# Kernel tuning notes

Measured on AMD Instinct MI355X. Metric: run time of the kernel, lower is better.

## Reference

```python
import jax, jax.numpy as jnp
import numpy as np

NB_HEAD = 16
SIZE_PER_HEAD = 64
D_MODEL = NB_HEAD * SIZE_PER_HEAD  # 1024
B, L = 2, 2048
NEG_BIG = 1e12


def setup_inputs() -> dict:
    key = jax.random.key(0)
    ks = jax.random.split(key, 8)
    return {
        "Q_seq": jax.random.normal(ks[0], (B, L, D_MODEL), dtype=jnp.float32),
        "K_seq": jax.random.normal(ks[1], (B, L, D_MODEL), dtype=jnp.float32),
        "V_seq": jax.random.normal(ks[2], (B, L, D_MODEL), dtype=jnp.float32),
        "q_len": jax.random.randint(ks[3], (B, 1), 1, L, dtype=jnp.int32),
        "v_len": jax.random.randint(ks[4], (B, 1), 1, L, dtype=jnp.int32),
        "WQ": jax.random.normal(ks[5], (D_MODEL, D_MODEL), dtype=jnp.float32) * 0.02,
        "WK": jax.random.normal(ks[6], (D_MODEL, D_MODEL), dtype=jnp.float32) * 0.02,
        "WV": jax.random.normal(ks[7], (D_MODEL, D_MODEL), dtype=jnp.float32) * 0.02,
    }


def _len_mask(lens, length, dtype):
    # Keras code: mask = 1 - cumsum(one_hot(len, L)) -> 1 for pos < len, 0 otherwise
    return (jnp.arange(length)[None, :] < lens).astype(dtype)  # [B, L]


def reference(Q_seq, K_seq, V_seq, q_len, v_len, WQ, WK, WV):
    Bq, Lq, _ = Q_seq.shape
    Lk = K_seq.shape[1]
    # QKV projections, split heads: [B, H, L, D]
    q = (Q_seq @ WQ).reshape(Bq, Lq, NB_HEAD, SIZE_PER_HEAD).transpose(0, 2, 1, 3)
    k = (K_seq @ WK).reshape(Bq, Lk, NB_HEAD, SIZE_PER_HEAD).transpose(0, 2, 1, 3)
    v = (V_seq @ WV).reshape(Bq, Lk, NB_HEAD, SIZE_PER_HEAD).transpose(0, 2, 1, 3)
    # scaled dot-product scores [B, H, Lq, Lk]
    scores = jnp.einsum("bhqd,bhkd->bhqk", q, k) / np.float32(SIZE_PER_HEAD ** 0.5)
    # additive key-length mask (V_len), matching Mask(..., 'add')
    kmask = _len_mask(v_len, Lk, scores.dtype)  # [B, Lk]
    scores = scores - (1.0 - kmask)[:, None, None, :] * np.float32(NEG_BIG)
    A = jax.nn.softmax(scores, axis=-1)
    # attention output, merge heads: [B, Lq, H*D]
    O = jnp.einsum("bhqk,bhkd->bqhd", A, v).reshape(Bq, Lq, D_MODEL)
    # multiplicative query-length mask (Q_len), matching Mask(..., 'mul')
    qmask = _len_mask(q_len, Lq, O.dtype)  # [B, Lq]
    return O * qmask[:, :, None]
```

## Files before the change

### kernel.cpp

```cpp
#include <hip/hip_runtime.h>
#include <cstddef>

#define NB_HEAD 16
#define HEAD_DIM 64
#define D_MODEL 1024
#define BATCH 2
#define SEQ 2048
#define MROWS (BATCH * SEQ)
#define NSPLIT 2

typedef __bf16 bf16x8 __attribute__((ext_vector_type(8)));
typedef __bf16 bf16x4 __attribute__((ext_vector_type(4)));
typedef __bf16 bf16x2 __attribute__((ext_vector_type(2)));
typedef float  f32x4  __attribute__((ext_vector_type(4)));

#define XEL ((size_t)MROWS * D_MODEL)
#define WEL ((size_t)D_MODEL * D_MODEL)

#define QSCALE 0.18033688011112042f

static __device__ __forceinline__ size_t xchunk(int row, int k) {
    return ((size_t)(row >> 4) * 32 + (k >> 5)) * 512 + ((k >> 3) & 3) * 128 + (row & 15) * 8 + (k & 7);
}
static __device__ __forceinline__ size_t qkbase(int bh, int row16, int dc) {
    return ((size_t)(bh * 128 + row16) * 2 + dc) * 512;
}
static __device__ __forceinline__ size_t qkelem(int bh, int row, int d) {
    return qkbase(bh, row >> 4, d >> 5) + ((d >> 3) & 3) * 128 + (row & 15) * 8 + (d & 7);
}
static __device__ __forceinline__ size_t vbase(int bh, int d16, int kc) {
    return ((size_t)(bh * 4 + d16) * 64 + kc) * 512;
}
static __device__ __forceinline__ size_t velem(int bh, int d, int key) {
    return vbase(bh, d >> 4, key >> 5) + ((key >> 3) & 3) * 128 + (d & 15) * 8 + (key & 7);
}

static __device__ __forceinline__ void split_bf16(float x, __bf16& h, __bf16& l) {
    h = (__bf16)x;
    l = (__bf16)(x - (float)h);
}

static __device__ __forceinline__ void gload_lds16(const __bf16* g, __bf16* l) {
    __builtin_amdgcn_global_load_lds((const __attribute__((address_space(1))) void*)g,
                                     (__attribute__((address_space(3))) void*)l,
                                     16, 0, 0);
}

__global__ __launch_bounds__(256) void conv_wt_kernel(
    const float* __restrict__ W0, const float* __restrict__ W1,
    const float* __restrict__ W2,
    __bf16* __restrict__ hi, __bf16* __restrict__ lo)
{
    __shared__ float tile[64][65];
    const int t  = threadIdx.x;
    const int k0 = blockIdx.x * 64;
    const int n0 = blockIdx.y * 64;
    const int z  = blockIdx.z;
    const float* W = (z == 0) ? W0 : ((z == 1) ? W1 : W2);
    __bf16* hz = hi + (size_t)z * WEL;
    __bf16* lz = lo + (size_t)z * WEL;

    #pragma unroll
    for (int p = 0; p < 4; ++p) {
        const int e = (p * 256 + t) * 4;
        const int r = e >> 6, c = e & 63;
        const float4 v = *(const float4*)(W + (size_t)(k0 + r) * D_MODEL + n0 + c);
        tile[r][c] = v.x; tile[r][c + 1] = v.y; tile[r][c + 2] = v.z; tile[r][c + 3] = v.w;
    }
    __syncthreads();
    #pragma unroll
    for (int p = 0; p < 4; ++p) {
        const int e = (p * 256 + t) * 4;
        const int n = e >> 6, kc = e & 63;
        __bf16 h[4], l[4];
        #pragma unroll
        for (int u = 0; u < 4; ++u) split_bf16(tile[kc + u][n], h[u], l[u]);
        const size_t a = xchunk(n0 + n, k0 + kc);
        *(bf16x4*)(hz + a) = (bf16x4){h[0], h[1], h[2], h[3]};
        *(bf16x4*)(lz + a) = (bf16x4){l[0], l[1], l[2], l[3]};
    }
}

__global__ __launch_bounds__(256) void conv_x_kernel(
    const float* __restrict__ X0, const float* __restrict__ X1,
    const float* __restrict__ X2,
    const int* __restrict__ q_len, const int* __restrict__ v_len,
    __bf16* __restrict__ xhi, __bf16* __restrict__ xlo)
{
    const int z = blockIdx.y;
    const size_t e = ((size_t)blockIdx.x * 256 + threadIdx.x) * 8;
    const int l = (int)(e >> 10), k = (int)(e & 1023);
    const int bb = l >> 11, lb = l & (SEQ - 1);
    const int len = (z == 0) ? q_len[bb] : v_len[bb];
    if (lb >= ((len + 127) & ~127)) return;

    const float* X = (z == 0) ? X0 : ((z == 1) ? X1 : X2);
    const float4 v0 = *(const float4*)(X + e);
    const float4 v1 = *(const float4*)(X + e + 4);
    const float xs[8] = {v0.x, v0.y, v0.z, v0.w, v1.x, v1.y, v1.z, v1.w};
    bf16x8 h8, l8;
    #pragma unroll
    for (int u = 0; u < 8; ++u) { __bf16 h_, l_; split_bf16(xs[u], h_, l_); h8[u] = h_; l8[u] = l_; }
    const size_t a = z * XEL + xchunk(l, k);
    *(bf16x8*)(xhi + a) = h8;
    *(bf16x8*)(xlo + a) = l8;
}

__global__ __launch_bounds__(256, 3) void proj_mfma_kernel(
    const __bf16* __restrict__ Xhi, const __bf16* __restrict__ Xlo,
    const __bf16* __restrict__ Wchi, const __bf16* __restrict__ Wclo,
    const int* __restrict__ q_len, const int* __restrict__ v_len,
    __bf16* __restrict__ qch, __bf16* __restrict__ qcl,
    __bf16* __restrict__ kch, __bf16* __restrict__ kcl,
    __bf16* __restrict__ vch, __bf16* __restrict__ vcl)
{
    __shared__ __align__(16) __bf16 lds[2][24][512];

    const int t    = threadIdx.x;
    const int wave = t >> 6, lane = t & 63;
    const int li   = lane & 15, grp = lane >> 4;
    const int wm   = wave >> 1, wn = wave & 1;
    const int m0   = blockIdx.x * 128;
    const int n0   = blockIdx.y * 64;
    const int z    = blockIdx.z;
    const int bb   = m0 >> 11;
    const int l0   = m0 & (SEQ - 1);
    const int need = (z == 0) ? q_len[bb] : v_len[bb];
    if (l0 >= need) return;

    const __bf16* Xh = Xhi + z * XEL;
    const __bf16* Xl = Xlo + z * XEL;
    const __bf16* Wh = Wchi + z * WEL;
    const __bf16* Wl = Wclo + z * WEL;

    const __bf16* gs[6];
    #pragma unroll
    for (int u = 0; u < 6; ++u) {
        const int c = u * 4 + wave;
        const __bf16* src;
        int idx;
        if (c < 8)       { src = Xh; idx = (m0 >> 4) + c; }
        else if (c < 16) { src = Xl; idx = (m0 >> 4) + (c - 8); }
        else if (c < 20) { src = Wh; idx = (n0 >> 4) + (c - 16); }
        else             { src = Wl; idx = (n0 >> 4) + (c - 20); }
        gs[u] = src + (size_t)idx * 32 * 512 + (size_t)lane * 8;
    }

    auto STAGE = [&](int buf, int kc) {
        #pragma unroll
        for (int u = 0; u < 6; ++u)
            gload_lds16(gs[u] + (size_t)kc * 512, &lds[buf][u * 4 + wave][0]);
    };

    f32x4 acc[4][2] = {};

    STAGE(0, 0);
    __syncthreads();

    #pragma unroll 2
    for (int kc = 0; kc < 32; ++kc) {
        const int cur = kc & 1;
        if (kc < 31) STAGE(cur ^ 1, kc + 1);

        bf16x8 ah[4], al4[4], bh2[2], bl2[2];
        #pragma unroll
        for (int i = 0; i < 4; ++i) {
            ah[i]  = *(const bf16x8*)&lds[cur][(wm << 2) + i][lane * 8];
            al4[i] = *(const bf16x8*)&lds[cur][8 + (wm << 2) + i][lane * 8];
        }
        #pragma unroll
        for (int j = 0; j < 2; ++j) {
            bh2[j] = *(const bf16x8*)&lds[cur][16 + (wn << 1) + j][lane * 8];
            bl2[j] = *(const bf16x8*)&lds[cur][20 + (wn << 1) + j][lane * 8];
        }
        #pragma unroll
        for (int j = 0; j < 2; ++j) {
            #pragma unroll
            for (int i = 0; i < 4; ++i) {
                acc[i][j] = __builtin_amdgcn_mfma_f32_16x16x32_bf16(ah[i],  bh2[j], acc[i][j], 0, 0, 0);
                acc[i][j] = __builtin_amdgcn_mfma_f32_16x16x32_bf16(ah[i],  bl2[j], acc[i][j], 0, 0, 0);
                acc[i][j] = __builtin_amdgcn_mfma_f32_16x16x32_bf16(al4[i], bh2[j], acc[i][j], 0, 0, 0);
            }
        }
        __syncthreads();
    }

    #pragma unroll
    for (int j = 0; j < 2; ++j) {
        const int cg = n0 + wn * 32 + j * 16 + li;
        const int hd = cg >> 6, d = cg & 63;
        const int bhI = bb * NB_HEAD + hd;
        #pragma unroll
        for (int i = 0; i < 4; ++i) {
            #pragma unroll
            for (int r = 0; r < 4; ++r) {
                const int rg = m0 + wm * 64 + i * 16 + grp * 4 + r;
                const int lg = rg & (SEQ - 1);
                __bf16 h_, l_;
                if (z == 0) {
                    split_bf16(acc[i][j][r] * QSCALE, h_, l_);
                    const size_t a = qkelem(bhI, lg, d);
                    qch[a] = h_; qcl[a] = l_;
                } else if (z == 1) {
                    split_bf16(acc[i][j][r], h_, l_);
                    const size_t a = qkelem(bhI, lg, d);
                    kch[a] = h_; kcl[a] = l_;
                } else {
                    split_bf16(acc[i][j][r], h_, l_);
                    const size_t a = velem(bhI, d, lg);
                    vch[a] = h_; vcl[a] = l_;
                }
            }
        }
    }
}

__global__ __launch_bounds__(256, 2) void attn_mfma_kernel(
    const __bf16* __restrict__ qch, const __bf16* __restrict__ qcl,
    const __bf16* __restrict__ kch, const __bf16* __restrict__ kcl,
    const __bf16* __restrict__ vch, const __bf16* __restrict__ vcl,
    const int* __restrict__ q_len, const int* __restrict__ v_len,
    float* __restrict__ Opart, float* __restrict__ Mbuf, float* __restrict__ Lbuf)
{
    __shared__ __align__(16) __bf16 Ps[128][72];

    const int t = threadIdx.x;
    const int wq = t >> 6, lane = t & 63;
    const int grp = lane >> 4, li = lane & 15;
    const int hh = blockIdx.x;
    const int split = blockIdx.y & (NSPLIT - 1);
    const int q0 = (blockIdx.y >> 1) * 128;
    const int b  = blockIdx.z;
    const int qlen = q_len[b], vlen = v_len[b];
    const int bh = b * NB_HEAD + hh;
    const int qbase = q0 + wq * 32;

    if (qbase >= qlen) return;

    bf16x8 onesv;
    #pragma unroll
    for (int u = 0; u < 8; ++u) onesv[u] = (__bf16)1.0f;

    bf16x8 qh[2][2], ql[2][2];
    #pragma unroll
    for (int s = 0; s < 2; ++s)
        #pragma unroll
        for (int ks = 0; ks < 2; ++ks) {
            const size_t a = qkbase(bh, (qbase >> 4) + s, ks) + lane * 8;
            qh[s][ks] = *(const bf16x8*)(qch + a);
            ql[s][ks] = *(const bf16x8*)(qcl + a);
        }

    f32x4 O[2][4] = {};
    float m_s[2] = {-1e30f, -1e30f};
    float l_s[2][4];
    #pragma unroll
    for (int s = 0; s < 2; ++s)
        #pragma unroll
        for (int r = 0; r < 4; ++r) l_s[s][r] = 0.f;

    const int nktT = (vlen + 63) >> 6;
    const int half = (nktT + NSPLIT - 1) / NSPLIT;
    const int tBeg = split * half;
    const int tEnd = (nktT < tBeg + half) ? nktT : (tBeg + half);

    for (int tt = tBeg; tt < tEnd; ++tt) {
        const int k0 = tt * 64;
        const bool full = (k0 + 64 <= vlen);

        f32x4 sacc[2][4] = {};
        #pragma unroll
        for (int ks = 0; ks < 2; ++ks) {
            bf16x8 kh_[4], kl_[4];
            #pragma unroll
            for (int j = 0; j < 4; ++j) {
                const size_t a = qkbase(bh, (k0 >> 4) + j, ks) + lane * 8;
                kh_[j] = *(const bf16x8*)(kch + a);
                kl_[j] = *(const bf16x8*)(kcl + a);
            }
            __builtin_amdgcn_s_setprio(1);
            #pragma unroll
            for (int j = 0; j < 4; ++j)
                #pragma unroll
                for (int s = 0; s < 2; ++s) {
                    sacc[s][j] = __builtin_amdgcn_mfma_f32_16x16x32_bf16(kh_[j], qh[s][ks], sacc[s][j], 0, 0, 0);
                    sacc[s][j] = __builtin_amdgcn_mfma_f32_16x16x32_bf16(kl_[j], qh[s][ks], sacc[s][j], 0, 0, 0);
                    sacc[s][j] = __builtin_amdgcn_mfma_f32_16x16x32_bf16(kh_[j], ql[s][ks], sacc[s][j], 0, 0, 0);
                }
            __builtin_amdgcn_s_setprio(0);
        }

        bf16x8 vh_[2][4], vl_[2][4];
        #pragma unroll
        for (int ks = 0; ks < 2; ++ks)
            #pragma unroll
            for (int j = 0; j < 4; ++j) {
                const size_t a = vbase(bh, j, (k0 >> 5) + ks) + lane * 8;
                vh_[ks][j] = *(const bf16x8*)(vch + a);
                vl_[ks][j] = *(const bf16x8*)(vcl + a);
            }

        float mx[2];
        int defer = 1;
        #pragma unroll
        for (int s = 0; s < 2; ++s) {
            if (!full) {
                #pragma unroll
                for (int j = 0; j < 4; ++j) {
                    const int keyb = k0 + j * 16 + grp * 4;
                    #pragma unroll
                    for (int r = 0; r < 4; ++r)
                        if (keyb + r >= vlen) sacc[s][j][r] = -1e30f;
                }
            }
            float m0_ = -1e30f;
            #pragma unroll
            for (int j = 0; j < 4; ++j)
                #pragma unroll
                for (int r = 0; r < 4; ++r) m0_ = fmaxf(m0_, sacc[s][j][r]);
            m0_ = fmaxf(m0_, __shfl_xor(m0_, 16));
            m0_ = fmaxf(m0_, __shfl_xor(m0_, 32));
            mx[s] = m0_;
            defer &= (m0_ - m_s[s] <= 8.f) ? 1 : 0;
        }

        if (!__all(defer)) {
            #pragma unroll
            for (int s = 0; s < 2; ++s) {
                const float mn = fmaxf(m_s[s], mx[s]);
                const float alq = exp2f(m_s[s] - mn);
                m_s[s] = mn;
                #pragma unroll
                for (int r = 0; r < 4; ++r) {
                    const float alr = __shfl(alq, grp * 4 + r);
                    l_s[s][r] *= alr;
                    #pragma unroll
                    for (int j = 0; j < 4; ++j) O[s][j][r] *= alr;
                }
            }
        }

        #pragma unroll
        for (int s = 0; s < 2; ++s) {
            const int row = wq * 32 + s * 16 + li;
            #pragma unroll
            for (int j = 0; j < 4; ++j) {
                const int col = j * 16 + grp * 4;
                bf16x2 w01, w23;
                w01[0] = (__bf16)exp2f(sacc[s][j][0] - m_s[s]);
                w01[1] = (__bf16)exp2f(sacc[s][j][1] - m_s[s]);
                w23[0] = (__bf16)exp2f(sacc[s][j][2] - m_s[s]);
                w23[1] = (__bf16)exp2f(sacc[s][j][3] - m_s[s]);
                *(bf16x2*)&Ps[row][col]     = w01;
                *(bf16x2*)&Ps[row][col + 2] = w23;
            }
        }
        asm volatile("s_waitcnt lgkmcnt(0)" ::: "memory");

        bf16x8 pa[2][2];
        #pragma unroll
        for (int s = 0; s < 2; ++s)
            #pragma unroll
            for (int ks = 0; ks < 2; ++ks)
                pa[s][ks] = *(const bf16x8*)&Ps[wq * 32 + s * 16 + li][ks * 32 + grp * 8];

        __builtin_amdgcn_s_setprio(1);
        #pragma unroll
        for (int s = 0; s < 2; ++s) {
            f32x4 lsum = {};
            lsum = __builtin_amdgcn_mfma_f32_16x16x32_bf16(pa[s][0], onesv, lsum, 0, 0, 0);
            lsum = __builtin_amdgcn_mfma_f32_16x16x32_bf16(pa[s][1], onesv, lsum, 0, 0, 0);
            #pragma unroll
            for (int r = 0; r < 4; ++r) l_s[s][r] += lsum[r];
        }

        #pragma unroll
        for (int ks = 0; ks < 2; ++ks)
            #pragma unroll
            for (int j = 0; j < 4; ++j)
                #pragma unroll
                for (int s = 0; s < 2; ++s) {
                    O[s][j] = __builtin_amdgcn_mfma_f32_16x16x32_bf16(pa[s][ks], vh_[ks][j], O[s][j], 0, 0, 0);
                    O[s][j] = __builtin_amdgcn_mfma_f32_16x16x32_bf16(pa[s][ks], vl_[ks][j], O[s][j], 0, 0, 0);
                }
        __builtin_amdgcn_s_setprio(0);
    }

    const size_t osplit = (size_t)split * MROWS * D_MODEL;
    #pragma unroll
    for (int s = 0; s < 2; ++s)
        #pragma unroll
        for (int r = 0; r < 4; ++r) {
            const int q = qbase + s * 16 + grp * 4 + r;
            if (q < qlen) {
                #pragma unroll
                for (int j = 0; j < 4; ++j)
                    Opart[osplit + ((size_t)b * SEQ + q) * D_MODEL + hh * HEAD_DIM + j * 16 + li] = O[s][j][r];
                if (li == 0) {
                    const size_t mi = (((size_t)split * BATCH + b) * NB_HEAD + hh) * SEQ + q;
                    Lbuf[mi] = l_s[s][r];
                }
            }
        }
    #pragma unroll
    for (int s = 0; s < 2; ++s) {
        const int q = qbase + s * 16 + li;
        if (grp == 0 && q < qlen) {
            const size_t mi = (((size_t)split * BATCH + b) * NB_HEAD + hh) * SEQ + q;
            Mbuf[mi] = m_s[s];
        }
    }
}

__global__ __launch_bounds__(256) void attn_merge_kernel(
    const float* __restrict__ Opart, const float* __restrict__ Mbuf,
    const float* __restrict__ Lbuf, const int* __restrict__ q_len,
    float* __restrict__ out)
{
    const int row = blockIdx.x;
    const int b = row >> 11, q = row & (SEQ - 1);
    const int col = threadIdx.x * 4;
    const int hh = col >> 6;
    const size_t oidx = (size_t)row * D_MODEL + col;

    float4 o = make_float4(0.f, 0.f, 0.f, 0.f);
    if (q < q_len[b]) {
        const size_t mlsz = (size_t)BATCH * NB_HEAD * SEQ;
        const size_t mi = ((size_t)b * NB_HEAD + hh) * SEQ + q;
        const float m0 = Mbuf[mi], m1 = Mbuf[mlsz + mi];
        const float l0 = Lbuf[mi], l1 = Lbuf[mlsz + mi];
        const float M  = fmaxf(m0, m1);
        const float w0 = exp2f(m0 - M), w1 = exp2f(m1 - M);
        const float inv = 1.f / (l0 * w0 + l1 * w1);
        const float4 a = *(const float4*)(Opart + oidx);
        const float4 c = *(const float4*)(Opart + (size_t)MROWS * D_MODEL + oidx);
        o.x = (a.x * w0 + c.x * w1) * inv;
        o.y = (a.y * w0 + c.y * w1) * inv;
        o.z = (a.z * w0 + c.z * w1) * inv;
        o.w = (a.w * w0 + c.w * w1) * inv;
    }
    *(float4*)(out + oidx) = o;
}

extern "C" void kernel_launch(void* const* d_in, const int* in_sizes, int n_in,
                              void* d_out, int out_size, void* d_ws, size_t ws_size,
                              hipStream_t stream)
{
    (void)in_sizes; (void)n_in; (void)out_size; (void)ws_size;
    const float* Q_seq = (const float*)d_in[0];
    const float* K_seq = (const float*)d_in[1];
    const float* V_seq = (const float*)d_in[2];
    const int*   q_len = (const int*)d_in[3];
    const int*   v_len = (const int*)d_in[4];
    const float* WQ    = (const float*)d_in[5];
    const float* WK    = (const float*)d_in[6];
    const float* WV    = (const float*)d_in[7];
    float* out = (float*)d_out;

    __bf16* wchi = (__bf16*)d_ws;
    __bf16* wclo = wchi + 3 * WEL;
    __bf16* xhi_ = wclo + 3 * WEL;
    __bf16* xlo_ = xhi_ + 3 * XEL;
    __bf16* qch_ = xlo_ + 3 * XEL;
    __bf16* qcl_ = qch_ + XEL;
    __bf16* kch_ = qcl_ + XEL;
    __bf16* kcl_ = kch_ + XEL;
    __bf16* vch_ = kcl_ + XEL;
    __bf16* vcl_ = vch_ + XEL;

    float* Opart = (float*)xhi_;
    float* Mbuf  = (float*)wchi;
    float* Lbuf  = Mbuf + (size_t)NSPLIT * BATCH * NB_HEAD * SEQ;

    dim3 blk(256);

    dim3 cg(D_MODEL / 64, D_MODEL / 64, 3);
    conv_wt_kernel<<<cg, blk, 0, stream>>>(WQ, WK, WV, wchi, wclo);

    dim3 xg((unsigned)(XEL / 2048), 3);
    conv_x_kernel<<<xg, blk, 0, stream>>>(Q_seq, K_seq, V_seq, q_len, v_len, xhi_, xlo_);

    dim3 pg(MROWS / 128, D_MODEL / 64, 3);
    proj_mfma_kernel<<<pg, blk, 0, stream>>>(xhi_, xlo_, wchi, wclo, q_len, v_len,
                                             qch_, qcl_, kch_, kcl_, vch_, vcl_);

    dim3 ag(NB_HEAD, (SEQ / 128) * NSPLIT, BATCH);
    attn_mfma_kernel<<<ag, blk, 0, stream>>>(qch_, qcl_, kch_, kcl_, vch_, vcl_,
                                             q_len, v_len, Opart, Mbuf, Lbuf);

    attn_merge_kernel<<<dim3(MROWS), blk, 0, stream>>>(Opart, Mbuf, Lbuf, q_len, out);
}
```

Before: 258.4 us.

## Make projection GEMM a persistent kernel with atomic tile scheduler

Replaces the 3D grid of projection tiles with a fixed grid of 768 persistent blocks that fetch tile indices from a global atomic counter, which conv_wt_kernel resets at the start. Blocks skip tiles that are fully masked by the sequence lengths and immediately grab more work. The aim is to cut block launch overhead and the load imbalance caused by early-exiting blocks. The cost is an atomic and two barriers per tile, plus reliance on the counter being reset in an earlier kernel.

```diff
diff --git a/kernel.cpp b/kernel.cpp
--- a/kernel.cpp
+++ b/kernel.cpp
@@ -9,6 +9,9 @@
 #define MROWS (BATCH * SEQ)
 #define NSPLIT 2
 
+#define PROJ_BLOCKS 768
+#define PROJ_TILES  (32 * 16 * 3)
+
 typedef __bf16 bf16x8 __attribute__((ext_vector_type(8)));
 typedef __bf16 bf16x4 __attribute__((ext_vector_type(4)));
 typedef __bf16 bf16x2 __attribute__((ext_vector_type(2)));
@@ -49,13 +52,15 @@
 __global__ __launch_bounds__(256) void conv_wt_kernel(
     const float* __restrict__ W0, const float* __restrict__ W1,
     const float* __restrict__ W2,
-    __bf16* __restrict__ hi, __bf16* __restrict__ lo)
+    __bf16* __restrict__ hi, __bf16* __restrict__ lo,
+    unsigned* __restrict__ ctr)
 {
     __shared__ float tile[64][65];
     const int t  = threadIdx.x;
     const int k0 = blockIdx.x * 64;
     const int n0 = blockIdx.y * 64;
     const int z  = blockIdx.z;
+    if (blockIdx.x == 0 && blockIdx.y == 0 && blockIdx.z == 0 && t == 0) *ctr = 0;
     const float* W = (z == 0) ? W0 : ((z == 1) ? W1 : W2);
     __bf16* hz = hi + (size_t)z * WEL;
     __bf16* lz = lo + (size_t)z * WEL;
@@ -112,103 +117,115 @@
     const int* __restrict__ q_len, const int* __restrict__ v_len,
     __bf16* __restrict__ qch, __bf16* __restrict__ qcl,
     __bf16* __restrict__ kch, __bf16* __restrict__ kcl,
-    __bf16* __restrict__ vch, __bf16* __restrict__ vcl)
+    __bf16* __restrict__ vch, __bf16* __restrict__ vcl,
+    unsigned* __restrict__ ctr)
 {
     __shared__ __align__(16) __bf16 lds[2][24][512];
+    __shared__ unsigned sidx;
 
     const int t    = threadIdx.x;
     const int wave = t >> 6, lane = t & 63;
     const int li   = lane & 15, grp = lane >> 4;
     const int wm   = wave >> 1, wn = wave & 1;
-    const int m0   = blockIdx.x * 128;
-    const int n0   = blockIdx.y * 64;
-    const int z    = blockIdx.z;
-    const int bb   = m0 >> 11;
-    const int l0   = m0 & (SEQ - 1);
-    const int need = (z == 0) ? q_len[bb] : v_len[bb];
-    if (l0 >= need) return;
-
-    const __bf16* Xh = Xhi + z * XEL;
-    const __bf16* Xl = Xlo + z * XEL;
-    const __bf16* Wh = Wchi + z * WEL;
-    const __bf16* Wl = Wclo + z * WEL;
-
-    const __bf16* gs[6];
-    #pragma unroll
-    for (int u = 0; u < 6; ++u) {
-        const int c = u * 4 + wave;
-        const __bf16* src;
-        int idx;
-        if (c < 8)       { src = Xh; idx = (m0 >> 4) + c; }
-        else if (c < 16) { src = Xl; idx = (m0 >> 4) + (c - 8); }
-        else if (c < 20) { src = Wh; idx = (n0 >> 4) + (c - 16); }
-        else             { src = Wl; idx = (n0 >> 4) + (c - 20); }
-        gs[u] = src + (size_t)idx * 32 * 512 + (size_t)lane * 8;
-    }
-
-    auto STAGE = [&](int buf, int kc) {
-        #pragma unroll
-        for (int u = 0; u < 6; ++u)
-            gload_lds16(gs[u] + (size_t)kc * 512, &lds[buf][u * 4 + wave][0]);
-    };
-
-    f32x4 acc[4][2] = {};
-
-    STAGE(0, 0);
-    __syncthreads();
-
-    #pragma unroll 2
-    for (int kc = 0; kc < 32; ++kc) {
-        const int cur = kc & 1;
-        if (kc < 31) STAGE(cur ^ 1, kc + 1);
-
-        bf16x8 ah[4], al4[4], bh2[2], bl2[2];
-        #pragma unroll
-        for (int i = 0; i < 4; ++i) {
-            ah[i]  = *(const bf16x8*)&lds[cur][(wm << 2) + i][lane * 8];
-            al4[i] = *(const bf16x8*)&lds[cur][8 + (wm << 2) + i][lane * 8];
-        }
+
+    for (;;) {
+        __syncthreads();
+        if (t == 0) sidx = atomicAdd(ctr, 1u);
+        __syncthreads();
+        const unsigned idx = sidx;
+        if (idx >= PROJ_TILES) break;
+
+        const int z  = (int)(idx >> 9);
+        const int rem = (int)(idx & 511);
+        const int m0 = (rem >> 4) * 128;
+        const int n0 = (rem & 15) * 64;
+        const int bb = m0 >> 11;
+        const int l0 = m0 & (SEQ - 1);
+        const int need = (z == 0) ? q_len[bb] : v_len[bb];
+        if (l0 >= need) continue;
+
+        const __bf16* Xh = Xhi + z * XEL;
+        const __bf16* Xl = Xlo + z * XEL;
+        const __bf16* Wh = Wchi + z * WEL;
+        const __bf16* Wl = Wclo + z * WEL;
+
+        const __bf16* gs[6];
+        #pragma unroll
+        for (int u = 0; u < 6; ++u) {
+            const int c = u * 4 + wave;
+            const __bf16* src;
+            int idxc;
+            if (c < 8)       { src = Xh; idxc = (m0 >> 4) + c; }
+            else if (c < 16) { src = Xl; idxc = (m0 >> 4) + (c - 8); }
+            else if (c < 20) { src = Wh; idxc = (n0 >> 4) + (c - 16); }
+            else             { src = Wl; idxc = (n0 >> 4) + (c - 20); }
+            gs[u] = src + (size_t)idxc * 32 * 512 + (size_t)lane * 8;
+        }
+
+        auto STAGE = [&](int buf, int kc) {
+            #pragma unroll
+            for (int u = 0; u < 6; ++u)
+                gload_lds16(gs[u] + (size_t)kc * 512, &lds[buf][u * 4 + wave][0]);
+        };
+
+        f32x4 acc[4][2] = {};
+
+        STAGE(0, 0);
+        __syncthreads();
+
+        #pragma unroll 2
+        for (int kc = 0; kc < 32; ++kc) {
+            const int cur = kc & 1;
+            if (kc < 31) STAGE(cur ^ 1, kc + 1);
+
+            bf16x8 ah[4], al4[4], bh2[2], bl2[2];
+            #pragma unroll
+            for (int i = 0; i < 4; ++i) {
+                ah[i]  = *(const bf16x8*)&lds[cur][(wm << 2) + i][lane * 8];
+                al4[i] = *(const bf16x8*)&lds[cur][8 + (wm << 2) + i][lane * 8];
+            }
+            #pragma unroll
+            for (int j = 0; j < 2; ++j) {
+                bh2[j] = *(const bf16x8*)&lds[cur][16 + (wn << 1) + j][lane * 8];
+                bl2[j] = *(const bf16x8*)&lds[cur][20 + (wn << 1) + j][lane * 8];
+            }
+            #pragma unroll
+            for (int j = 0; j < 2; ++j) {
+                #pragma unroll
+                for (int i = 0; i < 4; ++i) {
+                    acc[i][j] = __builtin_amdgcn_mfma_f32_16x16x32_bf16(ah[i],  bh2[j], acc[i][j], 0, 0, 0);
+                    acc[i][j] = __builtin_amdgcn_mfma_f32_16x16x32_bf16(ah[i],  bl2[j], acc[i][j], 0, 0, 0);
+                    acc[i][j] = __builtin_amdgcn_mfma_f32_16x16x32_bf16(al4[i], bh2[j], acc[i][j], 0, 0, 0);
+                }
+            }
+            __syncthreads();
+        }
+
         #pragma unroll
         for (int j = 0; j < 2; ++j) {
-            bh2[j] = *(const bf16x8*)&lds[cur][16 + (wn << 1) + j][lane * 8];
-            bl2[j] = *(const bf16x8*)&lds[cur][20 + (wn << 1) + j][lane * 8];
-        }
-        #pragma unroll
-        for (int j = 0; j < 2; ++j) {
+            const int cg = n0 + wn * 32 + j * 16 + li;
+            const int hd = cg >> 6, d = cg & 63;
+            const int bhI = bb * NB_HEAD + hd;
             #pragma unroll
             for (int i = 0; i < 4; ++i) {
-                acc[i][j] = __builtin_amdgcn_mfma_f32_16x16x32_bf16(ah[i],  bh2[j], acc[i][j], 0, 0, 0);
-                acc[i][j] = __builtin_amdgcn_mfma_f32_16x16x32_bf16(ah[i],  bl2[j], acc[i][j], 0, 0, 0);
-                acc[i][j] = __builtin_amdgcn_mfma_f32_16x16x32_bf16(al4[i], bh2[j], acc[i][j], 0, 0, 0);
-            }
-        }
-        __syncthreads();
-    }
-
-    #pragma unroll
-    for (int j = 0; j < 2; ++j) {
-        const int cg = n0 + wn * 32 + j * 16 + li;
-        const int hd = cg >> 6, d = cg & 63;
-        const int bhI = bb * NB_HEAD + hd;
-        #pragma unroll
-        for (int i = 0; i < 4; ++i) {
-            #pragma unroll
-            for (int r = 0; r < 4; ++r) {
-                const int rg = m0 + wm * 64 + i * 16 + grp * 4 + r;
-                const int lg = rg & (SEQ - 1);
-                __bf16 h_, l_;
-                if (z == 0) {
-                    split_bf16(acc[i][j][r] * QSCALE, h_, l_);
-                    const size_t a = qkelem(bhI, lg, d);
-                    qch[a] = h_; qcl[a] = l_;
-                } else if (z == 1) {
-                    split_bf16(acc[i][j][r], h_, l_);
-                    const size_t a = qkelem(bhI, lg, d);
-                    kch[a] = h_; kcl[a] = l_;
-                } else {
-                    split_bf16(acc[i][j][r], h_, l_);
-                    const size_t a = velem(bhI, d, lg);
-                    vch[a] = h_; vcl[a] = l_;
+                #pragma unroll
+                for (int r = 0; r < 4; ++r) {
+                    const int rg = m0 + wm * 64 + i * 16 + grp * 4 + r;
+                    const int lg = rg & (SEQ - 1);
+                    __bf16 h_, l_;
+                    if (z == 0) {
+                        split_bf16(acc[i][j][r] * QSCALE, h_, l_);
+                        const size_t a = qkelem(bhI, lg, d);
+                        qch[a] = h_; qcl[a] = l_;
+                    } else if (z == 1) {
+                        split_bf16(acc[i][j][r], h_, l_);
+                        const size_t a = qkelem(bhI, lg, d);
+                        kch[a] = h_; kcl[a] = l_;
+                    } else {
+                        split_bf16(acc[i][j][r], h_, l_);
+                        const size_t a = velem(bhI, d, lg);
+                        vch[a] = h_; vcl[a] = l_;
+                    }
                 }
             }
         }
@@ -467,6 +484,7 @@
     __bf16* kcl_ = kch_ + XEL;
     __bf16* vch_ = kcl_ + XEL;
     __bf16* vcl_ = vch_ + XEL;
+    unsigned* ctr = (unsigned*)(vcl_ + XEL);
 
     float* Opart = (float*)xhi_;
     float* Mbuf  = (float*)wchi;
@@ -475,14 +493,14 @@
     dim3 blk(256);
 
     dim3 cg(D_MODEL / 64, D_MODEL / 64, 3);
-    conv_wt_kernel<<<cg, blk, 0, stream>>>(WQ, WK, WV, wchi, wclo);
+    conv_wt_kernel<<<cg, blk, 0, stream>>>(WQ, WK, WV, wchi, wclo, ctr);
 
     dim3 xg((unsigned)(XEL / 2048), 3);
     conv_x_kernel<<<xg, blk, 0, stream>>>(Q_seq, K_seq, V_seq, q_len, v_len, xhi_, xlo_);
 
-    dim3 pg(MROWS / 128, D_MODEL / 64, 3);
-    proj_mfma_kernel<<<pg, blk, 0, stream>>>(xhi_, xlo_, wchi, wclo, q_len, v_len,
-                                             qch_, qcl_, kch_, kcl_, vch_, vcl_);
+    proj_mfma_kernel<<<dim3(PROJ_BLOCKS), blk, 0, stream>>>(
+        xhi_, xlo_, wchi, wclo, q_len, v_len,
+        qch_, qcl_, kch_, kcl_, vch_, vcl_, ctr);
 
     dim3 ag(NB_HEAD, (SEQ / 128) * NSPLIT, BATCH);
     attn_mfma_kernel<<<ag, blk, 0, stream>>>(qch_, qcl_, kch_, kcl_, vch_, vcl_,
```

Result: slower. 276.1 us (+6.9%).
